# Performance work log

Hardware: AMD Instinct MI355X
Metric: run time of the kernel (lower is better)

The kernel has to match this reference:

```python
import jax, jax.numpy as jnp
import numpy as np

WINDOW_SIZE = 11
SIGMA = 1.5
C1 = 0.01 ** 2
C2 = 0.03 ** 2


def _gaussian_window(channels):
    # 1D gaussian, normalized, then outer product -> (C,1,K,K) depthwise kernel
    coords = np.arange(WINDOW_SIZE, dtype=np.float32) - WINDOW_SIZE // 2
    g = np.exp(-(coords ** 2) / (2.0 * SIGMA ** 2))
    g = g / g.sum()
    w2d = np.outer(g, g).astype(np.float32)  # (K,K)
    w = np.broadcast_to(w2d, (channels, 1, WINDOW_SIZE, WINDOW_SIZE))
    return jnp.asarray(w)


def _dw_conv(x, w):
    # depthwise conv, SAME-style padding = K//2 (matches conv2d(padding=K//2, groups=C))
    pad = WINDOW_SIZE // 2
    return jax.lax.conv_general_dilated(
        x, w,
        window_strides=(1, 1),
        padding=[(pad, pad), (pad, pad)],
        dimension_numbers=("NCHW", "OIHW", "NCHW"),
        feature_group_count=x.shape[1],
    )


def _ssim(img1, img2):
    w = _gaussian_window(img1.shape[1]).astype(img1.dtype)
    mu1 = _dw_conv(img1, w)
    mu2 = _dw_conv(img2, w)
    mu1_sq = mu1 * mu1
    mu2_sq = mu2 * mu2
    mu1_mu2 = mu1 * mu2
    sigma1_sq = _dw_conv(img1 * img1, w) - mu1_sq
    sigma2_sq = _dw_conv(img2 * img2, w) - mu2_sq
    sigma12 = _dw_conv(img1 * img2, w) - mu1_mu2
    ssim_map = ((2.0 * mu1_mu2 + C1) * (2.0 * sigma12 + C2)) / (
        (mu1_sq + mu2_sq + C1) * (sigma1_sq + sigma2_sq + C2)
    )
    return jnp.mean(ssim_map)


def setup_inputs() -> dict:
    key = jax.random.key(0)
    k1, k2 = jax.random.split(key)
    shape = (16, 3, 512, 512)
    r_low = jax.random.uniform(k1, shape, dtype=jnp.float32)
    r_high = jax.random.uniform(k2, shape, dtype=jnp.float32)
    return {"r_low": r_low, "r_high": r_high}


def reference(r_low, r_high):
    ssim_loss = 1.0 - _ssim(r_low, r_high)
    mse_loss = jnp.mean((r_low - r_high) ** 2)
    return ssim_loss + mse_loss
```

## Files before the change

### kernel.cpp

```cpp
#include <hip/hip_runtime.h>
#include <cmath>


#define HH 512
#define WW 512
#define TILE_H 64
#define TILE_W 32
#define NT (HH / TILE_H)
#define HB (TILE_H + 10)
#define LDW 33
#define NPLANES 48
#define CT (WW / TILE_W)
#define NBLOCKS (NPLANES * CT)

struct GW { float g[11]; };

typedef float v2f __attribute__((ext_vector_type(2)));

__global__ __launch_bounds__(256, 3)
void ssim_main(const float* __restrict__ img1, const float* __restrict__ img2,
               float* __restrict__ partial, GW gw)
{
    __shared__ float4 hbuf[HB][LDW];
    __shared__ float red[4];

    const int tid   = threadIdx.x;
    const int bx    = blockIdx.x;
    const int plane = blockIdx.y;
    const int col0  = bx * TILE_W;
    const float* p1 = img1 + (size_t)plane * (HH * WW);
    const float* p2 = img2 + (size_t)plane * (HH * WW);

    const int cg    = tid & 7;
    const int rs    = tid >> 3;
    const int cbase = col0 + 4 * cg - 8;
    const bool interiorCol = (bx > 0) && (bx < CT - 1);

    float local = 0.f;

    auto loadRow = [&](int grow, float4* x1, float4* x2) {
        const bool rowOK = (grow >= 0) && (grow < HH);
        const int growc = min(max(grow, 0), HH - 1);
        const float* r1 = p1 + (size_t)growc * WW;
        const float* r2 = p2 + (size_t)growc * WW;
        if (rowOK && interiorCol) {
            #pragma unroll
            for (int v = 0; v < 5; ++v) {
                x1[v] = *reinterpret_cast<const float4*>(r1 + cbase + 4 * v);
                x2[v] = *reinterpret_cast<const float4*>(r2 + cbase + 4 * v);
            }
        } else {
            #pragma unroll
            for (int v = 0; v < 5; ++v) {
                const int c0 = cbase + 4 * v;
                if (rowOK && c0 >= 0 && c0 + 4 <= WW) {
                    x1[v] = *reinterpret_cast<const float4*>(r1 + c0);
                    x2[v] = *reinterpret_cast<const float4*>(r2 + c0);
                } else {
                    x1[v] = make_float4(0.f, 0.f, 0.f, 0.f);
                    x2[v] = make_float4(0.f, 0.f, 0.f, 0.f);
                }
            }
        }
    };

    auto convStore = [&](int rl, const float4* x1v, const float4* x2v) {
        const float* x1 = reinterpret_cast<const float*>(x1v);
        const float* x2 = reinterpret_cast<const float*>(x2v);
        if (rl >= 5 && rl < 69) {
            #pragma unroll
            for (int i = 0; i < 4; ++i) {
                float d = x1[8 + i] - x2[8 + i];
                local += d * d;
            }
        }
        v2f acc01[4], acc23[4];
        #pragma unroll
        for (int i = 0; i < 4; ++i) {
            acc01[i] = (v2f){0.f, 0.f};
            acc23[i] = (v2f){0.f, 0.f};
        }
        #pragma unroll
        for (int e = 3; e <= 16; ++e) {
            float a  = x1[e], b = x2[e];
            v2f ab = (v2f){a, b};
            v2f t  = ab * ab;
            v2f vv = (v2f){t.x + t.y, a * b};
            #pragma unroll
            for (int i = 0; i < 4; ++i) {
                int j = e - 3 - i;
                if (j >= 0 && j < 11) {
                    float w = gw.g[j];
                    v2f wv = (v2f){w, w};
                    acc01[i] += wv * ab;
                    acc23[i] += wv * vv;
                }
            }
        }
        #pragma unroll
        for (int i = 0; i < 4; ++i)
            hbuf[rl][4 * cg + i] = make_float4(acc01[i].x, acc01[i].y,
                                               acc23[i].x, acc23[i].y);
    };

    const bool third = (rs < 10);

    {
        float4 xA1[5], xA2[5], xB1[5], xB2[5];
        loadRow(-5 + rs, xA1, xA2);
        loadRow(27 + rs, xB1, xB2);
        convStore(rs, xA1, xA2);
        if (third) loadRow(59 + rs, xA1, xA2);
        convStore(rs + 32, xB1, xB2);
        if (third) convStore(rs + 64, xA1, xA2);
    }

    float4 xP1[5], xP2[5];
    #pragma unroll 1
    for (int t = 0; t < NT; ++t) {
        const int row0 = t * TILE_H;
        __syncthreads();

        if (t + 1 < NT)
            loadRow(row0 + TILE_H - 5 + rs, xP1, xP2);

        {
            const int tx = tid & 31;
            const int rg = tid >> 5;
            v2f res01[8], res23[8];
            #pragma unroll
            for (int p = 0; p < 8; ++p) {
                res01[p] = (v2f){0.f, 0.f};
                res23[p] = (v2f){0.f, 0.f};
            }
            #pragma unroll
            for (int j = 0; j < 18; ++j) {
                float4 u = hbuf[rg * 8 + j][tx];
                v2f f01 = (v2f){u.x, u.y};
                v2f f23 = (v2f){u.z, u.w};
                #pragma unroll
                for (int p = 0; p < 8; ++p) {
                    int tt = j - p;
                    if (tt >= 0 && tt < 11) {
                        float w = gw.g[tt];
                        v2f wv = (v2f){w, w};
                        res01[p] += wv * f01;
                        res23[p] += wv * f23;
                    }
                }
            }
            const float C1c = 0.0001f, C2c = 0.0009f;
            #pragma unroll
            for (int p = 0; p < 8; ++p) {
                float mu1 = res01[p].x, mu2 = res01[p].y;
                float S   = res23[p].x, P   = res23[p].y;
                float m11 = mu1 * mu1, m22 = mu2 * mu2, m12 = mu1 * mu2;
                float num = (2.f * m12 + C1c) * (2.f * (P - m12) + C2c);
                float den = (m11 + m22 + C1c) * ((S - m11 - m22) + C2c);
                float inv = __builtin_amdgcn_rcpf(den);
                local -= num * inv;
            }
        }

        if (t + 1 < NT) {
            __syncthreads();
            const int nrow0 = row0 + TILE_H;
            float4 xB1[5], xB2[5];
            loadRow(nrow0 + 27 + rs, xB1, xB2);
            convStore(rs, xP1, xP2);
            if (third) loadRow(nrow0 + 59 + rs, xP1, xP2);
            convStore(rs + 32, xB1, xB2);
            if (third) convStore(rs + 64, xP1, xP2);
        }
    }

    #pragma unroll
    for (int off = 32; off > 0; off >>= 1) local += __shfl_down(local, off);
    if ((tid & 63) == 0) red[tid >> 6] = local;
    __syncthreads();
    if (tid == 0)
        partial[plane * CT + bx] = (red[0] + red[1]) + (red[2] + red[3]);
}

__global__ __launch_bounds__(256)
void ssim_finish(const float* __restrict__ partial, float* __restrict__ out)
{
    __shared__ float red[256];
    float s = 0.f;
    #pragma unroll
    for (int i = 0; i < NBLOCKS / 256; ++i)
        s += partial[i * 256 + threadIdx.x];
    red[threadIdx.x] = s;
    __syncthreads();
    for (int step = 128; step > 0; step >>= 1) {
        if ((int)threadIdx.x < step) red[threadIdx.x] += red[threadIdx.x + step];
        __syncthreads();
    }
    if (threadIdx.x == 0)
        out[0] = 1.0f + red[0] * (1.0f / 12582912.0f);
}

extern "C" void kernel_launch(void* const* d_in, const int* in_sizes, int n_in,
                              void* d_out, int out_size, void* d_ws, size_t ws_size,
                              hipStream_t stream)
{
    const float* r_low  = (const float*)d_in[0];
    const float* r_high = (const float*)d_in[1];
    float* out     = (float*)d_out;
    float* partial = (float*)d_ws;

    GW gw;
    {
        float s = 0.f;
        for (int i = 0; i < 11; ++i) {
            float c = (float)(i - 5);
            gw.g[i] = expf(-(c * c) / 4.5f);
            s += gw.g[i];
        }
        for (int i = 0; i < 11; ++i) gw.g[i] /= s;
    }

    dim3 grid(CT, NPLANES);
    ssim_main<<<grid, dim3(256), 0, stream>>>(r_low, r_high, partial, gw);
    ssim_finish<<<1, dim3(256), 0, stream>>>(partial, out);
}
```

Before: 150.7 us.

## Run vertical Gaussian pass on MFMA with transposed fp16 shared buffer

Recasts the vertical 11-tap convolution of the four horizontally filtered quantities (mu1, mu2, sum of squares, product) as 16x16x32 fp16 MFMA matrix multiplies against a banded Gaussian weight fragment. The intermediate shared buffer changes from row-major float4 to a transposed, padded fp16 layout so that B fragments load as contiguous 8-half vectors. This is meant to remove the large scalar FMA count of the vertical pass. In exchange, intermediates are rounded to fp16, which risks accuracy in the variance terms computed by subtraction. The horizontal pass now writes scattered 2-byte stores, which may add LDS bank conflicts.

```diff
diff --git a/kernel.cpp b/kernel.cpp
--- a/kernel.cpp
+++ b/kernel.cpp
@@ -8,7 +8,7 @@
 #define TILE_W 32
 #define NT (HH / TILE_H)
 #define HB (TILE_H + 10)
-#define LDW 33
+#define TPAD 88
 #define NPLANES 48
 #define CT (WW / TILE_W)
 #define NBLOCKS (NPLANES * CT)
@@ -16,13 +16,16 @@
 struct GW { float g[11]; };
 
 typedef float v2f __attribute__((ext_vector_type(2)));
+typedef _Float16 f16x8 __attribute__((ext_vector_type(8)));
+typedef float f32x4 __attribute__((ext_vector_type(4)));
 
 __global__ __launch_bounds__(256, 3)
 void ssim_main(const float* __restrict__ img1, const float* __restrict__ img2,
                float* __restrict__ partial, GW gw)
 {
-    __shared__ float4 hbuf[HB][LDW];
+    __shared__ _Float16 hbufT[128][TPAD];
     __shared__ float red[4];
+    __shared__ float gt[16];
 
     const int tid   = threadIdx.x;
     const int bx    = blockIdx.x;
@@ -36,7 +39,26 @@
     const int cbase = col0 + 4 * cg - 8;
     const bool interiorCol = (bx > 0) && (bx < CT - 1);
 
+    const int lane = tid & 63;
+    const int l15  = lane & 15;
+    const int lc   = lane >> 4;
+    const int wv   = tid >> 6;
+
     float local = 0.f;
+
+    if (tid < 16) gt[tid] = (tid < 11) ? gw.g[tid] : 0.f;
+    if (tid < 128) {
+        #pragma unroll
+        for (int s = HB; s < TPAD; ++s) hbufT[tid][s] = (_Float16)0.f;
+    }
+    __syncthreads();
+    f16x8 wfrag;
+    #pragma unroll
+    for (int j = 0; j < 8; ++j) {
+        int idx = 8 * lc + j - l15;
+        int ridx = (idx >= 0 && idx <= 10) ? idx : 11;
+        wfrag[j] = (_Float16)gt[ridx];
+    }
 
     auto loadRow = [&](int grow, float4* x1, float4* x2) {
         const bool rowOK = (grow >= 0) && (grow < HH);
@@ -91,16 +113,20 @@
                 int j = e - 3 - i;
                 if (j >= 0 && j < 11) {
                     float w = gw.g[j];
-                    v2f wv = (v2f){w, w};
-                    acc01[i] += wv * ab;
-                    acc23[i] += wv * vv;
-                }
-            }
-        }
-        #pragma unroll
-        for (int i = 0; i < 4; ++i)
-            hbuf[rl][4 * cg + i] = make_float4(acc01[i].x, acc01[i].y,
-                                               acc23[i].x, acc23[i].y);
+                    v2f wv2 = (v2f){w, w};
+                    acc01[i] += wv2 * ab;
+                    acc23[i] += wv2 * vv;
+                }
+            }
+        }
+        _Float16* hb = &hbufT[0][0] + (4 * cg) * TPAD + rl;
+        #pragma unroll
+        for (int i = 0; i < 4; ++i) {
+            hb[i * TPAD + 0 * 32 * TPAD] = (_Float16)acc01[i].x;
+            hb[i * TPAD + 1 * 32 * TPAD] = (_Float16)acc01[i].y;
+            hb[i * TPAD + 2 * 32 * TPAD] = (_Float16)acc23[i].x;
+            hb[i * TPAD + 3 * 32 * TPAD] = (_Float16)acc23[i].y;
+        }
     };
 
     const bool third = (rs < 10);
@@ -125,40 +151,29 @@
             loadRow(row0 + TILE_H - 5 + rs, xP1, xP2);
 
         {
-            const int tx = tid & 31;
-            const int rg = tid >> 5;
-            v2f res01[8], res23[8];
-            #pragma unroll
-            for (int p = 0; p < 8; ++p) {
-                res01[p] = (v2f){0.f, 0.f};
-                res23[p] = (v2f){0.f, 0.f};
-            }
-            #pragma unroll
-            for (int j = 0; j < 18; ++j) {
-                float4 u = hbuf[rg * 8 + j][tx];
-                v2f f01 = (v2f){u.x, u.y};
-                v2f f23 = (v2f){u.z, u.w};
+            const int m0 = wv * 16;
+            const float C1c = 0.0001f, C2c = 0.0009f;
+            #pragma unroll
+            for (int cb = 0; cb < 2; ++cb) {
+                f32x4 D[4];
                 #pragma unroll
-                for (int p = 0; p < 8; ++p) {
-                    int tt = j - p;
-                    if (tt >= 0 && tt < 11) {
-                        float w = gw.g[tt];
-                        v2f wv = (v2f){w, w};
-                        res01[p] += wv * f01;
-                        res23[p] += wv * f23;
-                    }
-                }
-            }
-            const float C1c = 0.0001f, C2c = 0.0009f;
-            #pragma unroll
-            for (int p = 0; p < 8; ++p) {
-                float mu1 = res01[p].x, mu2 = res01[p].y;
-                float S   = res23[p].x, P   = res23[p].y;
-                float m11 = mu1 * mu1, m22 = mu2 * mu2, m12 = mu1 * mu2;
-                float num = (2.f * m12 + C1c) * (2.f * (P - m12) + C2c);
-                float den = (m11 + m22 + C1c) * ((S - m11 - m22) + C2c);
-                float inv = __builtin_amdgcn_rcpf(den);
-                local -= num * inv;
+                for (int f = 0; f < 4; ++f) {
+                    const _Float16* src =
+                        &hbufT[f * 32 + cb * 16 + l15][m0 + 8 * lc];
+                    f16x8 bfrag = *reinterpret_cast<const f16x8*>(src);
+                    D[f] = __builtin_amdgcn_mfma_f32_16x16x32_f16(
+                        wfrag, bfrag, (f32x4){0.f, 0.f, 0.f, 0.f}, 0, 0, 0);
+                }
+                #pragma unroll
+                for (int r = 0; r < 4; ++r) {
+                    float mu1 = D[0][r], mu2 = D[1][r];
+                    float S   = D[2][r], P   = D[3][r];
+                    float m11 = mu1 * mu1, m22 = mu2 * mu2, m12 = mu1 * mu2;
+                    float num = (2.f * m12 + C1c) * (2.f * (P - m12) + C2c);
+                    float den = (m11 + m22 + C1c) * ((S - m11 - m22) + C2c);
+                    float inv = __builtin_amdgcn_rcpf(den);
+                    local -= num * inv;
+                }
             }
         }
 
```

After: 147.7 us. -2.0%, faster.
